# Optimization experiments

Hardware: AMD Instinct MI355X
Metric: run time of the kernel (lower is better)

Reference implementation:

```python
import jax, jax.numpy as jnp
import numpy as np

N_NODES = 100000
N_EDGES = 1600000
IN_CH, HID_CH, OUT_CH = 128, 128, 64


def setup_inputs() -> dict:
    key = jax.random.key(0)
    k_x, k_e, k1, k2, k3 = jax.random.split(key, 5)
    x = jax.random.normal(k_x, (N_NODES, IN_CH), dtype=jnp.float32)
    edge_index = jax.random.randint(k_e, (2, N_EDGES), 0, N_NODES, dtype=jnp.int64)
    # Glorot-ish init for the three GCNConv weight matrices (no bias).
    W1 = jax.random.normal(k1, (IN_CH, HID_CH), dtype=jnp.float32) / np.sqrt(IN_CH)
    W2 = jax.random.normal(k2, (HID_CH, HID_CH), dtype=jnp.float32) / np.sqrt(HID_CH)
    W3 = jax.random.normal(k3, (HID_CH, OUT_CH), dtype=jnp.float32) / np.sqrt(HID_CH)
    return {"x": x, "edge_index": edge_index, "W1": W1, "W2": W2, "W3": W3}


def _gcn_layer(x, src, dst, W):
    # GCNConv(normalize=False, bias=False): transform then sum-aggregate over edges.
    h = x @ W                      # [N, d_out]
    msgs = h[src]                  # [E, d_out] gather from source nodes
    return jax.ops.segment_sum(msgs, dst, num_segments=N_NODES)  # scatter-add to targets


def reference(x, edge_index, W1, W2, W3):
    src, dst = edge_index[0], edge_index[1]  # PyG flow: source_to_target
    h = _gcn_layer(x, src, dst, W1)
    h = _gcn_layer(h, src, dst, W2)
    h = _gcn_layer(h, src, dst, W3)
    return h  # [N, OUT_CH]
```

## Files before the change

### kernel.cpp

```cpp
#include <hip/hip_runtime.h>

#define N_NODES 100000
#define N_EDGES 1600000
#define CAP 48
#define NBUCK 256
#define NPB 391
#define SCAP 8192
#define EPB 4096

typedef unsigned int uint;
typedef unsigned short ushort;

__device__ __forceinline__ void fma4(float4& c, float s, const float4& w) {
    c.x += s * w.x; c.y += s * w.y; c.z += s * w.z; c.w += s * w.w;
}

__device__ __forceinline__ ushort bf16r(float f) {
    union { float f; uint u; } v; v.f = f;
    return (ushort)((v.u + 0x7fffu + ((v.u >> 16) & 1u)) >> 16);
}

struct alignas(16) GemmSmem {
    float Xs[128][36];
    float Ws[32][64];
};

template <typename OutT>
__device__ __forceinline__ void gemm64_block(GemmSmem& sm, int bid,
                                             const float* __restrict__ X,
                                             const float* __restrict__ W,
                                             OutT* __restrict__ H, int n) {
    const int tid  = threadIdx.x;
    const int row0 = bid * 128;
    const int rg   = tid >> 4;
    const int cg   = tid & 15;

    float4 acc0[8];
#pragma unroll
    for (int r = 0; r < 8; r++) acc0[r] = make_float4(0.f, 0.f, 0.f, 0.f);

    const int lr = tid >> 1;
    const int lh = tid & 1;
    int grow = row0 + lr; if (grow > n - 1) grow = n - 1;
    const float* gx_base = X + (size_t)grow * 128 + lh * 16;

    for (int k0 = 0; k0 < 128; k0 += 32) {
        const float* gx = gx_base + k0;
#pragma unroll
        for (int i = 0; i < 4; i++)
            *(float4*)&sm.Xs[lr][lh * 16 + 4 * i] = *(const float4*)(gx + 4 * i);
        const float4* gw = (const float4*)(W + (size_t)k0 * 64);
        float4* sw = (float4*)&sm.Ws[0][0];
#pragma unroll
        for (int i = 0; i < 2; i++) sw[tid + 256 * i] = gw[tid + 256 * i];
        __syncthreads();

#pragma unroll
        for (int kk = 0; kk < 32; kk += 4) {
            float4 w00 = *(const float4*)&sm.Ws[kk + 0][cg * 4];
            float4 w01 = *(const float4*)&sm.Ws[kk + 1][cg * 4];
            float4 w02 = *(const float4*)&sm.Ws[kk + 2][cg * 4];
            float4 w03 = *(const float4*)&sm.Ws[kk + 3][cg * 4];
#pragma unroll
            for (int r = 0; r < 8; r++) {
                float4 a = *(const float4*)&sm.Xs[rg * 8 + r][kk];
                fma4(acc0[r], a.x, w00);
                fma4(acc0[r], a.y, w01);
                fma4(acc0[r], a.z, w02);
                fma4(acc0[r], a.w, w03);
            }
        }
        __syncthreads();
    }

#pragma unroll
    for (int r = 0; r < 8; r++) {
        int row = row0 + rg * 8 + r;
        if (row < n) {
            if constexpr (sizeof(OutT) == 2) {
                ushort4 o0 = make_ushort4(bf16r(acc0[r].x), bf16r(acc0[r].y),
                                          bf16r(acc0[r].z), bf16r(acc0[r].w));
                *(ushort4*)&H[(size_t)row * 64 + cg * 4] = o0;
            } else {
                *(float4*)&H[(size_t)row * 64 + cg * 4] = *(float4*)&acc0[r];
            }
        }
    }
}

union BinWcSmem {
    struct { int ecnt[NBUCK]; int base[NBUCK]; int lcur[NBUCK]; } b;
    GemmSmem g;
};

__global__ void __launch_bounds__(256) bin_wc(const int* __restrict__ src,
                                              const int* __restrict__ dst,
                                              int* __restrict__ gcur,
                                              uint2* __restrict__ seg, int E,
                                              const float* __restrict__ W1,
                                              const float* __restrict__ W2,
                                              const float* __restrict__ W3,
                                              float* __restrict__ W23,
                                              float* __restrict__ Wc) {
    __shared__ BinWcSmem sh;
    if (blockIdx.x == gridDim.x - 1) {
        gemm64_block<float>(sh.g, 0, W2, W3, W23, 128);
        __syncthreads();
        gemm64_block<float>(sh.g, 0, W1, W23, Wc, 128);
        return;
    }
    const int t = threadIdx.x;
    sh.b.ecnt[t] = 0; sh.b.lcur[t] = 0;
    __syncthreads();
    const int e0 = blockIdx.x * EPB;
#pragma unroll
    for (int k = 0; k < EPB / 256; k++) {
        int i = e0 + k * 256 + t;
        if (i < E) atomicAdd(&sh.b.ecnt[dst[i] / NPB], 1);
    }
    __syncthreads();
    sh.b.base[t] = (sh.b.ecnt[t] > 0) ? atomicAdd(&gcur[t], sh.b.ecnt[t]) : 0;
    __syncthreads();
#pragma unroll
    for (int k = 0; k < EPB / 256; k++) {
        int i = e0 + k * 256 + t;
        if (i < E) {
            int d = dst[i];
            int b = d / NPB;
            int s = sh.b.base[b] + atomicAdd(&sh.b.lcur[b], 1);
            if (s < SCAP) seg[(size_t)b * SCAP + s] = make_uint2((uint)src[i], (uint)d);
        }
    }
}

union CsrGemmSmem {
    int lc[NPB];
    GemmSmem g;
};

__global__ void __launch_bounds__(256, 3) csr_gemm(const int* __restrict__ gcur,
                                                   const uint2* __restrict__ seg,
                                                   int* __restrict__ col,
                                                   int* __restrict__ cnt,
                                                   const float* __restrict__ X,
                                                   const float* __restrict__ Wc,
                                                   ushort* __restrict__ Y, int n) {
    __shared__ CsrGemmSmem sh;
    if (blockIdx.x < NBUCK) {
        const int b = blockIdx.x;
        const int t = threadIdx.x;
        for (int i = t; i < NPB; i += 256) sh.lc[i] = 0;
        __syncthreads();
        int m = gcur[b]; if (m > SCAP) m = SCAP;
        const uint2* sg = seg + (size_t)b * SCAP;
        const int node0 = b * NPB;
        for (int i = t; i < m; i += 256) {
            uint2 e = sg[i];
            int d = (int)e.y;
            int slot = atomicAdd(&sh.lc[d - node0], 1);
            if (slot < CAP) col[(size_t)d * CAP + slot] = (int)e.x;
        }
        __syncthreads();
        for (int i = t; i < NPB; i += 256) {
            int node = node0 + i;
            if (node < n) cnt[node] = (sh.lc[i] > CAP) ? CAP : sh.lc[i];
        }
    } else {
        gemm64_block<ushort>(sh.g, blockIdx.x - NBUCK, X, Wc, Y, n);
    }
}

__device__ __forceinline__ float2 bf2f(uint u) {
    union { uint u; float f; } a, b;
    a.u = u << 16; b.u = u & 0xffff0000u;
    return make_float2(a.f, b.f);
}

__device__ __forceinline__ void acc4(float4& acc, uint2 u,
                                     float2& lo, float2& hi) {
    lo = bf2f(u.x); hi = bf2f(u.y);
    (void)acc;
}

template <bool FINAL>
__global__ void __launch_bounds__(256) agg64(const uint2* __restrict__ T_in,
                                             const int* __restrict__ cnt,
                                             const int* __restrict__ col,
                                             void* __restrict__ T_out, int n) {
    int gid  = blockIdx.x * blockDim.x + threadIdx.x;
    int node = gid >> 4;
    int lane = gid & 15;
    if (node >= n) return;
    int m = cnt[node]; if (m > CAP) m = CAP;
    const int* cb = col + (size_t)node * CAP;
    float4 acc = make_float4(0.f, 0.f, 0.f, 0.f);
    int j = 0;
    for (; j + 8 <= m; j += 8) {
        int s0 = cb[j],     s1 = cb[j + 1], s2 = cb[j + 2], s3 = cb[j + 3];
        int s4 = cb[j + 4], s5 = cb[j + 5], s6 = cb[j + 6], s7 = cb[j + 7];
        uint2 u0 = T_in[(size_t)s0 * 16 + lane];
        uint2 u1 = T_in[(size_t)s1 * 16 + lane];
        uint2 u2 = T_in[(size_t)s2 * 16 + lane];
        uint2 u3 = T_in[(size_t)s3 * 16 + lane];
        uint2 u4 = T_in[(size_t)s4 * 16 + lane];
        uint2 u5 = T_in[(size_t)s5 * 16 + lane];
        uint2 u6 = T_in[(size_t)s6 * 16 + lane];
        uint2 u7 = T_in[(size_t)s7 * 16 + lane];
        float2 a0 = bf2f(u0.x), a1 = bf2f(u1.x), a2 = bf2f(u2.x), a3 = bf2f(u3.x);
        float2 a4 = bf2f(u4.x), a5 = bf2f(u5.x), a6 = bf2f(u6.x), a7 = bf2f(u7.x);
        float2 b0 = bf2f(u0.y), b1 = bf2f(u1.y), b2 = bf2f(u2.y), b3 = bf2f(u3.y);
        float2 b4 = bf2f(u4.y), b5 = bf2f(u5.y), b6 = bf2f(u6.y), b7 = bf2f(u7.y);
        acc.x += ((a0.x + a1.x) + (a2.x + a3.x)) + ((a4.x + a5.x) + (a6.x + a7.x));
        acc.y += ((a0.y + a1.y) + (a2.y + a3.y)) + ((a4.y + a5.y) + (a6.y + a7.y));
        acc.z += ((b0.x + b1.x) + (b2.x + b3.x)) + ((b4.x + b5.x) + (b6.x + b7.x));
        acc.w += ((b0.y + b1.y) + (b2.y + b3.y)) + ((b4.y + b5.y) + (b6.y + b7.y));
    }
    for (; j + 4 <= m; j += 4) {
        int s0 = cb[j], s1 = cb[j + 1], s2 = cb[j + 2], s3 = cb[j + 3];
        uint2 u0 = T_in[(size_t)s0 * 16 + lane];
        uint2 u1 = T_in[(size_t)s1 * 16 + lane];
        uint2 u2 = T_in[(size_t)s2 * 16 + lane];
        uint2 u3 = T_in[(size_t)s3 * 16 + lane];
        float2 a0 = bf2f(u0.x), a1 = bf2f(u1.x), a2 = bf2f(u2.x), a3 = bf2f(u3.x);
        float2 b0 = bf2f(u0.y), b1 = bf2f(u1.y), b2 = bf2f(u2.y), b3 = bf2f(u3.y);
        acc.x += (a0.x + a1.x) + (a2.x + a3.x);
        acc.y += (a0.y + a1.y) + (a2.y + a3.y);
        acc.z += (b0.x + b1.x) + (b2.x + b3.x);
        acc.w += (b0.y + b1.y) + (b2.y + b3.y);
    }
    for (; j < m; j++) {
        uint2 u = T_in[(size_t)cb[j] * 16 + lane];
        float2 a = bf2f(u.x), b = bf2f(u.y);
        acc.x += a.x; acc.y += a.y; acc.z += b.x; acc.w += b.y;
    }
    if (FINAL) {
        ((float4*)T_out)[(size_t)node * 16 + lane] = acc;
    } else {
        uint2 o;
        o.x = (uint)bf16r(acc.x) | ((uint)bf16r(acc.y) << 16);
        o.y = (uint)bf16r(acc.z) | ((uint)bf16r(acc.w) << 16);
        ((uint2*)T_out)[(size_t)node * 16 + lane] = o;
    }
}


static inline size_t align_up(size_t x, size_t a) { return (x + a - 1) & ~(a - 1); }

extern "C" void kernel_launch(void* const* d_in, const int* in_sizes, int n_in,
                              void* d_out, int out_size, void* d_ws, size_t ws_size,
                              hipStream_t stream) {
    const float* x  = (const float*)d_in[0];
    const int*   ei = (const int*)d_in[1];
    const float* W1 = (const float*)d_in[2];
    const float* W2 = (const float*)d_in[3];
    const float* W3 = (const float*)d_in[4];
    float* out = (float*)d_out;

    const int N = N_NODES;
    const int E = N_EDGES;
    const int* src = ei;
    const int* dst = ei + E;

    char* p = (char*)d_ws;
    int*    gcur = (int*)p;   p += align_up((size_t)NBUCK * 4, 256);
    int*    cnt  = (int*)p;   p += align_up((size_t)N * 4, 256);
    uint2*  seg  = (uint2*)p; p += align_up((size_t)NBUCK * SCAP * 8, 256);
    int*    col  = (int*)p;   p += align_up((size_t)N * CAP * 4, 256);
    float*  W23  = (float*)p; p += align_up((size_t)128 * 64 * 4, 256);
    float*  Wc   = (float*)p; p += align_up((size_t)128 * 64 * 4, 256);
    ushort* Y    = (ushort*)p; p += align_up((size_t)N * 64 * 2, 256);
    ushort* Za   = (ushort*)p; p += align_up((size_t)N * 64 * 2, 256);

    hipMemsetAsync(gcur, 0, (size_t)NBUCK * 4, stream);

    const int bin_blocks = (E + EPB - 1) / EPB;
    bin_wc<<<bin_blocks + 1, 256, 0, stream>>>(src, dst, gcur, seg, E,
                                               W1, W2, W3, W23, Wc);

    const int gemm_blocks = (N + 127) / 128;
    csr_gemm<<<NBUCK + gemm_blocks, 256, 0, stream>>>(gcur, seg, col, cnt,
                                                      x, Wc, Y, N);

    const int agg_blocks = (N * 16 + 255) / 256;
    agg64<false><<<agg_blocks, 256, 0, stream>>>((const uint2*)Y,  cnt, col, Za, N);
    agg64<false><<<agg_blocks, 256, 0, stream>>>((const uint2*)Za, cnt, col, Y,  N);
    agg64<true ><<<agg_blocks, 256, 0, stream>>>((const uint2*)Y,  cnt, col, out, N);
}
```

Baseline: 253.2 us.

## Split bf16 feature tables into four column slabs for cache-local aggregation

Stores the intermediate bf16 node features as four column slabs of 16 channels each (32 bytes per node) instead of one 128-byte row. The aggregation kernel now runs slab by slab, with 4 lanes per node and blocks grouped by slab. Each gather pass therefore touches a 3.2 MB table that fits in L2, rather than the full 12.8 MB table. In exchange, each node's neighbor indices are read four times and each gathered segment is only 32 bytes wide.

```diff
diff --git a/kernel.cpp b/kernel.cpp
--- a/kernel.cpp
+++ b/kernel.cpp
@@ -7,6 +7,8 @@
 #define NPB 391
 #define SCAP 8192
 #define EPB 4096
+#define NSPLIT 4
+#define BPS ((N_NODES * 4 + 255) / 256)
 
 typedef unsigned int uint;
 typedef unsigned short ushort;
@@ -78,9 +80,12 @@
         int row = row0 + rg * 8 + r;
         if (row < n) {
             if constexpr (sizeof(OutT) == 2) {
-                ushort4 o0 = make_ushort4(bf16r(acc0[r].x), bf16r(acc0[r].y),
-                                          bf16r(acc0[r].z), bf16r(acc0[r].w));
-                *(ushort4*)&H[(size_t)row * 64 + cg * 4] = o0;
+                uint2 o;
+                o.x = (uint)bf16r(acc0[r].x) | ((uint)bf16r(acc0[r].y) << 16);
+                o.y = (uint)bf16r(acc0[r].z) | ((uint)bf16r(acc0[r].w) << 16);
+                const int s = cg >> 2;
+                const int q = cg & 3;
+                *(uint2*)((uint*)H + ((size_t)s * N_NODES + row) * 8 + q * 2) = o;
             } else {
                 *(float4*)&H[(size_t)row * 64 + cg * 4] = *(float4*)&acc0[r];
             }
@@ -176,36 +181,33 @@
     return make_float2(a.f, b.f);
 }
 
-__device__ __forceinline__ void acc4(float4& acc, uint2 u,
-                                     float2& lo, float2& hi) {
-    lo = bf2f(u.x); hi = bf2f(u.y);
-    (void)acc;
-}
-
 template <bool FINAL>
-__global__ void __launch_bounds__(256) agg64(const uint2* __restrict__ T_in,
-                                             const int* __restrict__ cnt,
-                                             const int* __restrict__ col,
-                                             void* __restrict__ T_out, int n) {
-    int gid  = blockIdx.x * blockDim.x + threadIdx.x;
-    int node = gid >> 4;
-    int lane = gid & 15;
+__global__ void __launch_bounds__(256) agg64s(const uint2* __restrict__ T_in,
+                                              const int* __restrict__ cnt,
+                                              const int* __restrict__ col,
+                                              void* __restrict__ T_out, int n) {
+    const int b = blockIdx.x;
+    const int s = b / BPS;
+    const int idx = (b - s * BPS) * 256 + threadIdx.x;
+    const int node = idx >> 2;
+    const int lane = idx & 3;
     if (node >= n) return;
     int m = cnt[node]; if (m > CAP) m = CAP;
     const int* cb = col + (size_t)node * CAP;
+    const uint2* tb = T_in + ((size_t)s * n) * 4 + lane;
     float4 acc = make_float4(0.f, 0.f, 0.f, 0.f);
     int j = 0;
     for (; j + 8 <= m; j += 8) {
         int s0 = cb[j],     s1 = cb[j + 1], s2 = cb[j + 2], s3 = cb[j + 3];
         int s4 = cb[j + 4], s5 = cb[j + 5], s6 = cb[j + 6], s7 = cb[j + 7];
-        uint2 u0 = T_in[(size_t)s0 * 16 + lane];
-        uint2 u1 = T_in[(size_t)s1 * 16 + lane];
-        uint2 u2 = T_in[(size_t)s2 * 16 + lane];
-        uint2 u3 = T_in[(size_t)s3 * 16 + lane];
-        uint2 u4 = T_in[(size_t)s4 * 16 + lane];
-        uint2 u5 = T_in[(size_t)s5 * 16 + lane];
-        uint2 u6 = T_in[(size_t)s6 * 16 + lane];
-        uint2 u7 = T_in[(size_t)s7 * 16 + lane];
+        uint2 u0 = tb[(size_t)s0 * 4];
+        uint2 u1 = tb[(size_t)s1 * 4];
+        uint2 u2 = tb[(size_t)s2 * 4];
+        uint2 u3 = tb[(size_t)s3 * 4];
+        uint2 u4 = tb[(size_t)s4 * 4];
+        uint2 u5 = tb[(size_t)s5 * 4];
+        uint2 u6 = tb[(size_t)s6 * 4];
+        uint2 u7 = tb[(size_t)s7 * 4];
         float2 a0 = bf2f(u0.x), a1 = bf2f(u1.x), a2 = bf2f(u2.x), a3 = bf2f(u3.x);
         float2 a4 = bf2f(u4.x), a5 = bf2f(u5.x), a6 = bf2f(u6.x), a7 = bf2f(u7.x);
         float2 b0 = bf2f(u0.y), b1 = bf2f(u1.y), b2 = bf2f(u2.y), b3 = bf2f(u3.y);
@@ -217,10 +219,10 @@
     }
     for (; j + 4 <= m; j += 4) {
         int s0 = cb[j], s1 = cb[j + 1], s2 = cb[j + 2], s3 = cb[j + 3];
-        uint2 u0 = T_in[(size_t)s0 * 16 + lane];
-        uint2 u1 = T_in[(size_t)s1 * 16 + lane];
-        uint2 u2 = T_in[(size_t)s2 * 16 + lane];
-        uint2 u3 = T_in[(size_t)s3 * 16 + lane];
+        uint2 u0 = tb[(size_t)s0 * 4];
+        uint2 u1 = tb[(size_t)s1 * 4];
+        uint2 u2 = tb[(size_t)s2 * 4];
+        uint2 u3 = tb[(size_t)s3 * 4];
         float2 a0 = bf2f(u0.x), a1 = bf2f(u1.x), a2 = bf2f(u2.x), a3 = bf2f(u3.x);
         float2 b0 = bf2f(u0.y), b1 = bf2f(u1.y), b2 = bf2f(u2.y), b3 = bf2f(u3.y);
         acc.x += (a0.x + a1.x) + (a2.x + a3.x);
@@ -229,17 +231,17 @@
         acc.w += (b0.y + b1.y) + (b2.y + b3.y);
     }
     for (; j < m; j++) {
-        uint2 u = T_in[(size_t)cb[j] * 16 + lane];
-        float2 a = bf2f(u.x), b = bf2f(u.y);
-        acc.x += a.x; acc.y += a.y; acc.z += b.x; acc.w += b.y;
+        uint2 u = tb[(size_t)cb[j] * 4];
+        float2 a = bf2f(u.x), bb = bf2f(u.y);
+        acc.x += a.x; acc.y += a.y; acc.z += bb.x; acc.w += bb.y;
     }
     if (FINAL) {
-        ((float4*)T_out)[(size_t)node * 16 + lane] = acc;
+        ((float4*)T_out)[(size_t)node * 16 + s * 4 + lane] = acc;
     } else {
         uint2 o;
         o.x = (uint)bf16r(acc.x) | ((uint)bf16r(acc.y) << 16);
         o.y = (uint)bf16r(acc.z) | ((uint)bf16r(acc.w) << 16);
-        ((uint2*)T_out)[(size_t)node * 16 + lane] = o;
+        ((uint2*)T_out)[((size_t)s * n + node) * 4 + lane] = o;
     }
 }
 
@@ -281,8 +283,8 @@
     csr_gemm<<<NBUCK + gemm_blocks, 256, 0, stream>>>(gcur, seg, col, cnt,
                                                       x, Wc, Y, N);
 
-    const int agg_blocks = (N * 16 + 255) / 256;
-    agg64<false><<<agg_blocks, 256, 0, stream>>>((const uint2*)Y,  cnt, col, Za, N);
-    agg64<false><<<agg_blocks, 256, 0, stream>>>((const uint2*)Za, cnt, col, Y,  N);
-    agg64<true ><<<agg_blocks, 256, 0, stream>>>((const uint2*)Y,  cnt, col, out, N);
-}
+    const int agg_blocks = NSPLIT * BPS;
+    agg64s<false><<<agg_blocks, 256, 0, stream>>>((const uint2*)Y,  cnt, col, Za, N);
+    agg64s<false><<<agg_blocks, 256, 0, stream>>>((const uint2*)Za, cnt, col, Y,  N);
+    agg64s<true ><<<agg_blocks, 256, 0, stream>>>((const uint2*)Y,  cnt, col, out, N);
+}
```

After: 333.2 us. 31.6% more time.

## Overlap X·Wc GEMM with edge binning via flag-gated fused kernel; separate CSR build

Applied to the files above, without the earlier changes.

Moves the dense X·Wc GEMM into the first kernel alongside edge binning. Block 0 computes the folded weight Wc and publishes a release flag, and the GEMM blocks spin on that flag before starting. The CSR build becomes its own kernel using 1024-thread blocks per bucket, so it no longer shares a launch with the GEMM. This trades a cross-block spin-wait, which depends on block 0 being scheduled first, for running the GEMM concurrently with binning rather than with the CSR build.

```diff
diff --git a/kernel.cpp b/kernel.cpp
--- a/kernel.cpp
+++ b/kernel.cpp
@@ -7,6 +7,8 @@
 #define NPB 391
 #define SCAP 8192
 #define EPB 4096
+#define NBIN ((N_EDGES + EPB - 1) / EPB)
+#define NGEMM ((N_NODES + 127) / 128)
 
 typedef unsigned int uint;
 typedef unsigned short ushort;
@@ -88,85 +90,91 @@
     }
 }
 
-union BinWcSmem {
+union FusedASmem {
     struct { int ecnt[NBUCK]; int base[NBUCK]; int lcur[NBUCK]; } b;
     GemmSmem g;
 };
 
-__global__ void __launch_bounds__(256) bin_wc(const int* __restrict__ src,
-                                              const int* __restrict__ dst,
-                                              int* __restrict__ gcur,
-                                              uint2* __restrict__ seg, int E,
-                                              const float* __restrict__ W1,
-                                              const float* __restrict__ W2,
-                                              const float* __restrict__ W3,
-                                              float* __restrict__ W23,
-                                              float* __restrict__ Wc) {
-    __shared__ BinWcSmem sh;
-    if (blockIdx.x == gridDim.x - 1) {
+__global__ void __launch_bounds__(256, 3) fused_a(const int* __restrict__ src,
+                                                  const int* __restrict__ dst,
+                                                  int* __restrict__ gcur,
+                                                  uint2* __restrict__ seg, int E,
+                                                  const float* __restrict__ W1,
+                                                  const float* __restrict__ W2,
+                                                  const float* __restrict__ W3,
+                                                  float* __restrict__ W23,
+                                                  float* __restrict__ Wc,
+                                                  int* __restrict__ wcflag,
+                                                  const float* __restrict__ X,
+                                                  ushort* __restrict__ Y, int n) {
+    __shared__ FusedASmem sh;
+    const int bx = blockIdx.x;
+    if (bx == 0) {
         gemm64_block<float>(sh.g, 0, W2, W3, W23, 128);
         __syncthreads();
         gemm64_block<float>(sh.g, 0, W1, W23, Wc, 128);
+        __syncthreads();
+        if (threadIdx.x == 0) {
+            __threadfence();
+            __hip_atomic_store(wcflag, 1, __ATOMIC_RELEASE, __HIP_MEMORY_SCOPE_AGENT);
+        }
         return;
     }
+    if (bx <= NBIN) {
+        const int t = threadIdx.x;
+        sh.b.ecnt[t] = 0; sh.b.lcur[t] = 0;
+        __syncthreads();
+        const int e0 = (bx - 1) * EPB;
+#pragma unroll
+        for (int k = 0; k < EPB / 256; k++) {
+            int i = e0 + k * 256 + t;
+            if (i < E) atomicAdd(&sh.b.ecnt[dst[i] / NPB], 1);
+        }
+        __syncthreads();
+        sh.b.base[t] = (sh.b.ecnt[t] > 0) ? atomicAdd(&gcur[t], sh.b.ecnt[t]) : 0;
+        __syncthreads();
+#pragma unroll
+        for (int k = 0; k < EPB / 256; k++) {
+            int i = e0 + k * 256 + t;
+            if (i < E) {
+                int d = dst[i];
+                int b = d / NPB;
+                int s = sh.b.base[b] + atomicAdd(&sh.b.lcur[b], 1);
+                if (s < SCAP) seg[(size_t)b * SCAP + s] = make_uint2((uint)src[i], (uint)d);
+            }
+        }
+        return;
+    }
+    if (threadIdx.x == 0) {
+        while (!__hip_atomic_load(wcflag, __ATOMIC_ACQUIRE, __HIP_MEMORY_SCOPE_AGENT))
+            __builtin_amdgcn_s_sleep(16);
+    }
+    __syncthreads();
+    gemm64_block<ushort>(sh.g, bx - 1 - NBIN, X, Wc, Y, n);
+}
+
+__global__ void __launch_bounds__(1024) build_csr(const int* __restrict__ gcur,
+                                                  const uint2* __restrict__ seg,
+                                                  int* __restrict__ col,
+                                                  int* __restrict__ cnt, int n) {
+    __shared__ int lc[NPB];
+    const int b = blockIdx.x;
     const int t = threadIdx.x;
-    sh.b.ecnt[t] = 0; sh.b.lcur[t] = 0;
+    for (int i = t; i < NPB; i += 1024) lc[i] = 0;
     __syncthreads();
-    const int e0 = blockIdx.x * EPB;
-#pragma unroll
-    for (int k = 0; k < EPB / 256; k++) {
-        int i = e0 + k * 256 + t;
-        if (i < E) atomicAdd(&sh.b.ecnt[dst[i] / NPB], 1);
+    int m = gcur[b]; if (m > SCAP) m = SCAP;
+    const uint2* sg = seg + (size_t)b * SCAP;
+    const int node0 = b * NPB;
+    for (int i = t; i < m; i += 1024) {
+        uint2 e = sg[i];
+        int d = (int)e.y;
+        int slot = atomicAdd(&lc[d - node0], 1);
+        if (slot < CAP) col[(size_t)d * CAP + slot] = (int)e.x;
     }
     __syncthreads();
-    sh.b.base[t] = (sh.b.ecnt[t] > 0) ? atomicAdd(&gcur[t], sh.b.ecnt[t]) : 0;
-    __syncthreads();
-#pragma unroll
-    for (int k = 0; k < EPB / 256; k++) {
-        int i = e0 + k * 256 + t;
-        if (i < E) {
-            int d = dst[i];
-            int b = d / NPB;
-            int s = sh.b.base[b] + atomicAdd(&sh.b.lcur[b], 1);
-            if (s < SCAP) seg[(size_t)b * SCAP + s] = make_uint2((uint)src[i], (uint)d);
-        }
-    }
-}
-
-union CsrGemmSmem {
-    int lc[NPB];
-    GemmSmem g;
-};
-
-__global__ void __launch_bounds__(256, 3) csr_gemm(const int* __restrict__ gcur,
-                                                   const uint2* __restrict__ seg,
-                                                   int* __restrict__ col,
-                                                   int* __restrict__ cnt,
-                                                   const float* __restrict__ X,
-                                                   const float* __restrict__ Wc,
-                                                   ushort* __restrict__ Y, int n) {
-    __shared__ CsrGemmSmem sh;
-    if (blockIdx.x < NBUCK) {
-        const int b = blockIdx.x;
-        const int t = threadIdx.x;
-        for (int i = t; i < NPB; i += 256) sh.lc[i] = 0;
-        __syncthreads();
-        int m = gcur[b]; if (m > SCAP) m = SCAP;
-        const uint2* sg = seg + (size_t)b * SCAP;
-        const int node0 = b * NPB;
-        for (int i = t; i < m; i += 256) {
-            uint2 e = sg[i];
-            int d = (int)e.y;
-            int slot = atomicAdd(&sh.lc[d - node0], 1);
-            if (slot < CAP) col[(size_t)d * CAP + slot] = (int)e.x;
-        }
-        __syncthreads();
-        for (int i = t; i < NPB; i += 256) {
-            int node = node0 + i;
-            if (node < n) cnt[node] = (sh.lc[i] > CAP) ? CAP : sh.lc[i];
-        }
-    } else {
-        gemm64_block<ushort>(sh.g, blockIdx.x - NBUCK, X, Wc, Y, n);
+    for (int i = t; i < NPB; i += 1024) {
+        int node = node0 + i;
+        if (node < n) cnt[node] = (lc[i] > CAP) ? CAP : lc[i];
     }
 }
 
@@ -174,12 +182,6 @@
     union { uint u; float f; } a, b;
     a.u = u << 16; b.u = u & 0xffff0000u;
     return make_float2(a.f, b.f);
-}
-
-__device__ __forceinline__ void acc4(float4& acc, uint2 u,
-                                     float2& lo, float2& hi) {
-    lo = bf2f(u.x); hi = bf2f(u.y);
-    (void)acc;
 }
 
 template <bool FINAL>
@@ -262,7 +264,8 @@
     const int* dst = ei + E;
 
     char* p = (char*)d_ws;
-    int*    gcur = (int*)p;   p += align_up((size_t)NBUCK * 4, 256);
+    int*    gcur = (int*)p;   p += align_up((size_t)(NBUCK + 64) * 4, 256);
+    int*    wcflag = gcur + NBUCK;
     int*    cnt  = (int*)p;   p += align_up((size_t)N * 4, 256);
     uint2*  seg  = (uint2*)p; p += align_up((size_t)NBUCK * SCAP * 8, 256);
     int*    col  = (int*)p;   p += align_up((size_t)N * CAP * 4, 256);
@@ -271,15 +274,13 @@
     ushort* Y    = (ushort*)p; p += align_up((size_t)N * 64 * 2, 256);
     ushort* Za   = (ushort*)p; p += align_up((size_t)N * 64 * 2, 256);
 
-    hipMemsetAsync(gcur, 0, (size_t)NBUCK * 4, stream);
-
-    const int bin_blocks = (E + EPB - 1) / EPB;
-    bin_wc<<<bin_blocks + 1, 256, 0, stream>>>(src, dst, gcur, seg, E,
-                                               W1, W2, W3, W23, Wc);
-
-    const int gemm_blocks = (N + 127) / 128;
-    csr_gemm<<<NBUCK + gemm_blocks, 256, 0, stream>>>(gcur, seg, col, cnt,
-                                                      x, Wc, Y, N);
+    hipMemsetAsync(gcur, 0, (size_t)(NBUCK + 64) * 4, stream);
+
+    fused_a<<<1 + NBIN + NGEMM, 256, 0, stream>>>(src, dst, gcur, seg, E,
+                                                  W1, W2, W3, W23, Wc, wcflag,
+                                                  x, Y, N);
+
+    build_csr<<<NBUCK, 1024, 0, stream>>>(gcur, seg, col, cnt, N);
 
     const int agg_blocks = (N * 16 + 255) / 256;
     agg64<false><<<agg_blocks, 256, 0, stream>>>((const uint2*)Y,  cnt, col, Za, N);
```

Measured after the change: 291.8 us. 1.15x slower.
